# Kernel tuning notes

Measured on AMD Instinct MI355X. Metric: run time of the kernel, lower is better.

## Reference

```python
import jax, jax.numpy as jnp
import numpy as np

N = 50000        # total nodes (disjoint batch of graphs)
E = 800000       # total edges
F_IN = 8         # node feature dim
S = 6            # edge feature dim
H = 20           # ECC kernel-network hidden size (hidden_states)
N_OUT = 20       # ECC output channels (n_out=hidden_states)
G = 32           # GCN channels
D1 = 16          # first dense
N_GRAPHS = 512   # graphs in batch


def setup_inputs() -> dict:
    key = jax.random.key(0)
    ks = jax.random.split(key, 24)
    r = lambda k, sh, s: jax.random.normal(k, sh, dtype=jnp.float32) * s
    return {
        "x": r(ks[0], (N, F_IN), 1.0),
        "e": r(ks[1], (E, S), 1.0),
        "edge_index": jax.random.randint(ks[2], (2, E), 0, N, dtype=jnp.int32),
        "seg": jnp.sort(jax.random.randint(ks[3], (N,), 0, N_GRAPHS, dtype=jnp.int32)),
        # ECC kernel network: S -> H -> H -> F_IN*N_OUT
        "ecc_w1": r(ks[4], (S, H), 0.4), "ecc_b1": jnp.zeros((H,), jnp.float32),
        "ecc_w2": r(ks[5], (H, H), 0.2), "ecc_b2": jnp.zeros((H,), jnp.float32),
        "ecc_w3": r(ks[6], (H, F_IN * N_OUT), 0.2), "ecc_b3": jnp.zeros((F_IN * N_OUT,), jnp.float32),
        "ecc_root": r(ks[7], (F_IN, N_OUT), 0.3), "ecc_b": jnp.zeros((N_OUT,), jnp.float32),
        "gcn1_w": r(ks[8], (N_OUT, G), 0.2), "gcn1_b": jnp.zeros((G,), jnp.float32),
        "gcn2_w": r(ks[9], (G, G), 0.2), "gcn2_b": jnp.zeros((G,), jnp.float32),
        "d1_w": r(ks[10], (G, D1), 0.2), "d1_b": jnp.zeros((D1,), jnp.float32),
        "d2_w": r(ks[11], (D1, 1), 0.2), "d2_b": jnp.zeros((1,), jnp.float32),
    }


def reference(x, e, edge_index, seg,
              ecc_w1, ecc_b1, ecc_w2, ecc_b2, ecc_w3, ecc_b3, ecc_root, ecc_b,
              gcn1_w, gcn1_b, gcn2_w, gcn2_b, d1_w, d1_b, d2_w, d2_b):
    row, col = edge_index[0], edge_index[1]  # message col -> row

    # --- ECCConv: per-edge MLP produces an [F_IN, N_OUT] filter per edge ---
    h = jax.nn.relu(e @ ecc_w1 + ecc_b1)
    h = jax.nn.relu(h @ ecc_w2 + ecc_b2)
    w_edge = (h @ ecc_w3 + ecc_b3).reshape(E, F_IN, N_OUT)   # [E, F_in, F_out]
    msg = jnp.einsum('ef,efo->eo', x[col], w_edge)            # per-edge message
    agg = jax.ops.segment_sum(msg, row, num_segments=N)
    x1 = jax.nn.relu(agg + x @ ecc_root + ecc_b)              # root + bias + relu

    # --- GCN normalization from the edge list (A + I, symmetric norm) ---
    deg = jax.ops.segment_sum(jnp.ones((E,), x.dtype), row, num_segments=N) + 1.0
    dinv = jax.lax.rsqrt(deg)
    edge_norm = (dinv[row] * dinv[col])[:, None]
    self_norm = (dinv * dinv)[:, None]

    def gcn(hin, W, b):
        hw = hin @ W
        nmsg = jax.ops.segment_sum(edge_norm * hw[col], row, num_segments=N)
        return jax.nn.relu(nmsg + self_norm * hw + b)

    x2 = gcn(x1, gcn1_w, gcn1_b)
    x3 = gcn(x2, gcn2_w, gcn2_b)

    # --- GlobalSumPool over graph ids, then MLP head ---
    pooled = jax.ops.segment_sum(x3, seg, num_segments=N_GRAPHS)  # [n_graphs, G]
    out = (pooled @ d1_w + d1_b) @ d2_w + d2_b                    # [n_graphs, 1]
    return out
```

## Files before the change

kernel.cpp:

```cpp
#include <hip/hip_runtime.h>

#define S_DIM   6
#define H_DIM   20
#define F_INN   8
#define N_OUTC  20
#define G_DIM   32
#define D1_DIM  16
#define NGRAPH  512

__global__ __launch_bounds__(256) void loc_kernel(
    const int* __restrict__ ei, int E, int* __restrict__ cnt,
    int* __restrict__ loc)
{
    int i = blockIdx.x * 256 + threadIdx.x;
    if (i >= E) return;
    loc[i] = atomicAdd(&cnt[ei[i]], 1);
}

__global__ __launch_bounds__(256) void scanA_kernel(
    const int* __restrict__ deg, int N, int* __restrict__ bsum)
{
    int i = blockIdx.x * 256 + threadIdx.x;
    int v = (i < N) ? deg[i] : 0;
#pragma unroll
    for (int d = 1; d < 64; d <<= 1) v += __shfl_down(v, d, 64);
    __shared__ int ws[4];
    int wid = threadIdx.x >> 6;
    if ((threadIdx.x & 63) == 0) ws[wid] = v;
    __syncthreads();
    if (threadIdx.x == 0) bsum[blockIdx.x] = ws[0] + ws[1] + ws[2] + ws[3];
}

__global__ __launch_bounds__(256) void scanC_kernel(
    const int* __restrict__ deg, int N, const int* __restrict__ bsum, int nbl,
    int E, int* __restrict__ rowptr, float* __restrict__ dinv)
{
    __shared__ int ws[4];
    __shared__ int sboff;
    int t = threadIdx.x;

    {
        int v = (t < nbl && t < blockIdx.x) ? bsum[t] : 0;
#pragma unroll
        for (int d = 1; d < 64; d <<= 1) v += __shfl_down(v, d, 64);
        int wid = t >> 6;
        if ((t & 63) == 0) ws[wid] = v;
        __syncthreads();
        if (t == 0) sboff = ws[0] + ws[1] + ws[2] + ws[3];
        __syncthreads();
    }

    int i = blockIdx.x * 256 + t;
    int d0 = (i < N) ? deg[i] : 0;
    int v = d0;
#pragma unroll
    for (int d = 1; d < 64; d <<= 1) {
        int u = __shfl_up(v, d, 64);
        if ((t & 63) >= d) v += u;
    }
    __shared__ int ws2[4];
    int wid = t >> 6;
    if ((t & 63) == 63) ws2[wid] = v;
    __syncthreads();
    int woff = 0;
    for (int w = 0; w < wid; ++w) woff += ws2[w];
    if (i < N) {
        rowptr[i] = sboff + woff + v - d0;
        dinv[i] = rsqrtf((float)d0 + 1.0f);
    }
    if (blockIdx.x == 0 && t == 0) rowptr[N] = E;
}

__global__ __launch_bounds__(256) void build_kernel(
    const int* __restrict__ ei, int E, const int* __restrict__ rowptr,
    const int* __restrict__ loc,
    int* __restrict__ eid_at_slot, int* __restrict__ col_sorted)
{
    int i = blockIdx.x * 256 + threadIdx.x;
    if (i >= E) return;
    int p = rowptr[ei[i]] + loc[i];
    eid_at_slot[p] = i;
    col_sorted[p] = ei[E + i];
}

__global__ __launch_bounds__(256) void ecc_fused_kernel(
    const float* __restrict__ e, const float* __restrict__ x,
    const int* __restrict__ eid_at_slot, const int* __restrict__ col_sorted,
    const int* __restrict__ rowptr, int N, int E,
    const float* __restrict__ w1, const float* __restrict__ b1,
    const float* __restrict__ w2, const float* __restrict__ b2,
    const float* __restrict__ w3, const float* __restrict__ b3,
    float* __restrict__ agg)
{
    __shared__ float4 lmsg[5][257];
    __shared__ int rbounds[2];

    int t = threadIdx.x;
    int j0 = blockIdx.x * 256;
    int j = j0 + t;
    int jend = min(j0 + 256, E);

    if (t < 2) {
        int s = (t == 0) ? j0 : (jend - 1);
        int lo = 0, hi = N - 1;
        while (lo < hi) {
            int m = (lo + hi + 1) >> 1;
            if (rowptr[m] <= s) lo = m; else hi = m - 1;
        }
        rbounds[t] = lo;
    }

    if (j < E) {
        int i = eid_at_slot[j];
        int c = col_sorted[j];

        float ef[S_DIM];
#pragma unroll
        for (int s = 0; s < S_DIM; ++s) ef[s] = e[(size_t)i * S_DIM + s];

        float h1[H_DIM];
#pragma unroll
        for (int jj = 0; jj < H_DIM; ++jj) {
            float a = b1[jj];
#pragma unroll
            for (int s = 0; s < S_DIM; ++s) a = fmaf(ef[s], w1[s * H_DIM + jj], a);
            h1[jj] = fmaxf(a, 0.0f);
        }

        float h2[H_DIM];
#pragma unroll
        for (int jj = 0; jj < H_DIM; ++jj) {
            float a = b2[jj];
#pragma unroll
            for (int k = 0; k < H_DIM; ++k) a = fmaf(h1[k], w2[k * H_DIM + jj], a);
            h2[jj] = fmaxf(a, 0.0f);
        }

        const float4* xp = (const float4*)&x[(size_t)c * F_INN];
        float4 xa = xp[0], xb = xp[1];
        float xf[F_INN] = {xa.x, xa.y, xa.z, xa.w, xb.x, xb.y, xb.z, xb.w};

        float msg[N_OUTC];
#pragma unroll
        for (int o = 0; o < N_OUTC; ++o) msg[o] = 0.0f;

        for (int f = 0; f < F_INN; ++f) {
            float xv = xf[f];
#pragma unroll
            for (int o = 0; o < N_OUTC; ++o) {
                float w = b3[f * N_OUTC + o];
#pragma unroll
                for (int k = 0; k < H_DIM; ++k)
                    w = fmaf(h2[k], w3[k * (F_INN * N_OUTC) + f * N_OUTC + o], w);
                msg[o] = fmaf(xv, w, msg[o]);
            }
        }

        lmsg[0][t] = make_float4(msg[0],  msg[1],  msg[2],  msg[3]);
        lmsg[1][t] = make_float4(msg[4],  msg[5],  msg[6],  msg[7]);
        lmsg[2][t] = make_float4(msg[8],  msg[9],  msg[10], msg[11]);
        lmsg[3][t] = make_float4(msg[12], msg[13], msg[14], msg[15]);
        lmsg[4][t] = make_float4(msg[16], msg[17], msg[18], msg[19]);
    }
    __syncthreads();

    int r0 = rbounds[0], r1 = rbounds[1];
    int work = (r1 - r0 + 1) * 5;
    for (int w = t; w < work; w += 256) {
        int row = r0 + w / 5;
        int q = w - (w / 5) * 5;
        int a0 = rowptr[row], a1 = rowptr[row + 1];
        int s0 = max(a0, j0), s1 = min(a1, jend);
        float4 acc = make_float4(0.f, 0.f, 0.f, 0.f);
        for (int s = s0; s < s1; ++s) {
            float4 v = lmsg[q][s - j0];
            acc.x += v.x; acc.y += v.y; acc.z += v.z; acc.w += v.w;
        }
        float* dst = &agg[(size_t)row * N_OUTC + q * 4];
        if (a0 >= j0 && a1 <= jend) {
            *(float4*)dst = acc;
        } else {
            unsafeAtomicAdd(dst + 0, acc.x);
            unsafeAtomicAdd(dst + 1, acc.y);
            unsafeAtomicAdd(dst + 2, acc.z);
            unsafeAtomicAdd(dst + 3, acc.w);
        }
    }
}

__global__ __launch_bounds__(256) void node1_kernel(
    const float* __restrict__ agg, const float* __restrict__ x,
    const float* __restrict__ dinv, int N,
    const float* __restrict__ root, const float* __restrict__ eb,
    const float* __restrict__ g1w,
    float* __restrict__ hws1)
{
    int n = blockIdx.x * 256 + threadIdx.x;
    if (n >= N) return;

    const float4* xp = (const float4*)&x[(size_t)n * F_INN];
    float4 xa = xp[0], xb = xp[1];
    float xf[F_INN] = {xa.x, xa.y, xa.z, xa.w, xb.x, xb.y, xb.z, xb.w};

    float x1[N_OUTC];
#pragma unroll
    for (int o = 0; o < N_OUTC; ++o) {
        float a = agg[(size_t)n * N_OUTC + o] + eb[o];
#pragma unroll
        for (int f = 0; f < F_INN; ++f) a = fmaf(xf[f], root[f * N_OUTC + o], a);
        x1[o] = fmaxf(a, 0.0f);
    }

    float di = dinv[n];
    float4* hp = (float4*)&hws1[(size_t)n * G_DIM];
#pragma unroll
    for (int q = 0; q < G_DIM / 4; ++q) {
        float4 v;
        float* vv = &v.x;
#pragma unroll
        for (int u = 0; u < 4; ++u) {
            int g = q * 4 + u;
            float a = 0.0f;
#pragma unroll
            for (int o = 0; o < N_OUTC; ++o) a = fmaf(x1[o], g1w[o * G_DIM + g], a);
            vv[u] = a * di;
        }
        hp[q] = v;
    }
}

template<bool DO_MATMUL>
__global__ __launch_bounds__(256) void gcn_gather_kernel(
    const float* __restrict__ hws, const int* __restrict__ rowptr,
    const int* __restrict__ col_sorted, const float* __restrict__ dinv, int N,
    const float* __restrict__ bias, const float* __restrict__ w2,
    float* __restrict__ outbuf)
{
    __shared__ float x2s[32 * 33];
    __shared__ float w2s[G_DIM * G_DIM];

    int t = threadIdx.x;
    int nl = t >> 3;
    int q = t & 7;
    int n = blockIdx.x * 32 + nl;

    if (DO_MATMUL) {
        ((float4*)w2s)[t] = ((const float4*)w2)[t];
    }

    float4 xo = make_float4(0.f, 0.f, 0.f, 0.f);
    float di = 0.0f;
    if (n < N) {
        di = dinv[n];
        int j0 = rowptr[n], j1 = rowptr[n + 1];
        float4 s = *(const float4*)&hws[(size_t)n * G_DIM + q * 4];
        for (int j = j0; j < j1; ++j) {
            int c = col_sorted[j];
            float4 v = *(const float4*)&hws[(size_t)c * G_DIM + q * 4];
            s.x += v.x; s.y += v.y; s.z += v.z; s.w += v.w;
        }
        const float4 b4 = *(const float4*)&bias[q * 4];
        xo.x = fmaxf(fmaf(di, s.x, b4.x), 0.0f);
        xo.y = fmaxf(fmaf(di, s.y, b4.y), 0.0f);
        xo.z = fmaxf(fmaf(di, s.z, b4.z), 0.0f);
        xo.w = fmaxf(fmaf(di, s.w, b4.w), 0.0f);
    }

    if (DO_MATMUL) {
        x2s[nl * 33 + q * 4 + 0] = xo.x;
        x2s[nl * 33 + q * 4 + 1] = xo.y;
        x2s[nl * 33 + q * 4 + 2] = xo.z;
        x2s[nl * 33 + q * 4 + 3] = xo.w;
        __syncthreads();
        if (n < N) {
            float a0 = 0.f, a1 = 0.f, a2 = 0.f, a3 = 0.f;
            const float* xr = &x2s[nl * 33];
#pragma unroll
            for (int g = 0; g < G_DIM; ++g) {
                float xv = xr[g];
                a0 = fmaf(xv, w2s[g * G_DIM + q * 4 + 0], a0);
                a1 = fmaf(xv, w2s[g * G_DIM + q * 4 + 1], a1);
                a2 = fmaf(xv, w2s[g * G_DIM + q * 4 + 2], a2);
                a3 = fmaf(xv, w2s[g * G_DIM + q * 4 + 3], a3);
            }
            *(float4*)&outbuf[(size_t)n * G_DIM + q * 4] =
                make_float4(a0 * di, a1 * di, a2 * di, a3 * di);
        }
    } else {
        if (n < N)
            *(float4*)&outbuf[(size_t)n * G_DIM + q * 4] = xo;
    }
}

__global__ __launch_bounds__(256) void pool_head_kernel(
    const float* __restrict__ x3, const int* __restrict__ seg, int N,
    const float* __restrict__ d1w, const float* __restrict__ d1b,
    const float* __restrict__ d2w, const float* __restrict__ d2b,
    float* __restrict__ out)
{
    __shared__ float red[8][G_DIM];
    __shared__ float pvec[G_DIM];
    __shared__ int bounds[2];
    int g = blockIdx.x;
    int t = threadIdx.x;
    if (t < 2) {
        int target = g + t;
        int lo = 0, hi = N;
        while (lo < hi) {
            int m = (lo + hi) >> 1;
            if (seg[m] < target) lo = m + 1; else hi = m;
        }
        bounds[t] = lo;
    }
    __syncthreads();
    int n0 = bounds[0], n1 = bounds[1];
    int ch = t & (G_DIM - 1);
    int slice = t >> 5;
    float a = 0.0f;
    for (int n = n0 + slice; n < n1; n += 8)
        a += x3[(size_t)n * G_DIM + ch];
    red[slice][ch] = a;
    __syncthreads();
    if (slice == 0) {
        float s = red[0][ch];
#pragma unroll
        for (int k = 1; k < 8; ++k) s += red[k][ch];
        pvec[ch] = s;
    }
    __syncthreads();
    if (t < D1_DIM) {
        float tj = d1b[t];
#pragma unroll
        for (int gg = 0; gg < G_DIM; ++gg)
            tj = fmaf(pvec[gg], d1w[gg * D1_DIM + t], tj);
        float acc = tj * d2w[t];
#pragma unroll
        for (int d = 1; d < D1_DIM; d <<= 1) acc += __shfl_down(acc, d, 64);
        if (t == 0) out[g] = acc + d2b[0];
    }
}

extern "C" void kernel_launch(void* const* d_in, const int* in_sizes, int n_in,
                              void* d_out, int out_size, void* d_ws, size_t ws_size,
                              hipStream_t stream)
{
    const float* x    = (const float*)d_in[0];
    const float* e    = (const float*)d_in[1];
    const int*   ei   = (const int*)d_in[2];
    const int*   seg  = (const int*)d_in[3];
    const float* w1   = (const float*)d_in[4];
    const float* b1   = (const float*)d_in[5];
    const float* w2   = (const float*)d_in[6];
    const float* b2   = (const float*)d_in[7];
    const float* w3   = (const float*)d_in[8];
    const float* b3   = (const float*)d_in[9];
    const float* root = (const float*)d_in[10];
    const float* eb   = (const float*)d_in[11];
    const float* g1w  = (const float*)d_in[12];
    const float* g1b  = (const float*)d_in[13];
    const float* g2w  = (const float*)d_in[14];
    const float* g2b  = (const float*)d_in[15];
    const float* d1w  = (const float*)d_in[16];
    const float* d1b  = (const float*)d_in[17];
    const float* d2w  = (const float*)d_in[18];
    const float* d2b  = (const float*)d_in[19];

    const int N = in_sizes[3];
    const int E = in_sizes[1] / S_DIM;
    float* out = (float*)d_out;

    const int nbl = (N + 255) / 256;
    const int ebl = (E + 255) / 256;

    char* ws = (char*)d_ws;
    size_t off = 0;
    auto alloc = [&](size_t elems) -> char* {
        char* p = ws + off;
        off += ((elems * 4 + 15) & ~(size_t)15);
        return p;
    };
    int*   cnt        = (int*)  alloc(N);
    float* agg        = (float*)alloc((size_t)N * N_OUTC);
    size_t zero_bytes = off;
    int*   rowptr     = (int*)  alloc(N + 1);
    int*   bsum       = (int*)  alloc(nbl);
    float* dinv       = (float*)alloc(N);
    int*   loc        = (int*)  alloc(E);
    int*   eid_at_slot= (int*)  alloc(E);
    int*   col_sorted = (int*)  alloc(E);
    float* hws1       = (float*)alloc((size_t)N * G_DIM);
    float* hws2       = (float*)alloc((size_t)N * G_DIM);
    float* x3         = (float*)alloc((size_t)N * G_DIM);
    (void)ws_size;

    hipMemsetAsync(d_ws, 0, zero_bytes, stream);

    loc_kernel<<<ebl, 256, 0, stream>>>(ei, E, cnt, loc);
    scanA_kernel<<<nbl, 256, 0, stream>>>(cnt, N, bsum);
    scanC_kernel<<<nbl, 256, 0, stream>>>(cnt, N, bsum, nbl, E, rowptr, dinv);
    build_kernel<<<ebl, 256, 0, stream>>>(ei, E, rowptr, loc, eid_at_slot, col_sorted);
    ecc_fused_kernel<<<ebl, 256, 0, stream>>>(e, x, eid_at_slot, col_sorted,
                                              rowptr, N, E,
                                              w1, b1, w2, b2, w3, b3, agg);
    node1_kernel<<<nbl, 256, 0, stream>>>(agg, x, dinv, N, root, eb, g1w, hws1);
    gcn_gather_kernel<true><<<(N + 31) / 32, 256, 0, stream>>>(
        hws1, rowptr, col_sorted, dinv, N, g1b, g2w, hws2);
    gcn_gather_kernel<false><<<(N + 31) / 32, 256, 0, stream>>>(
        hws2, rowptr, col_sorted, dinv, N, g2b, nullptr, x3);
    pool_head_kernel<<<NGRAPH, 256, 0, stream>>>(x3, seg, N, d1w, d1b, d2w, d2b, out);
}
```

Measured before the change: 314.6 us.

## Compute ECC edge-filter contraction with bf16 MFMA instead of scalar FMAs

The per-edge third MLP layer and the x-weighted contraction are reformulated as one GEMM over the outer product h2⊗x (K=160, plus 8 bias terms) against a reshaped w3/b3 matrix. This matrix is run on 16x16x32 bf16 MFMA instructions. The weight B-fragments are staged through shared memory in bf16, and the message buffer is reused for the segmented reduction. This is meant to remove roughly 3200 scalar FMAs per edge, which dominated the kernel. The cost is bf16 rounding of the activations and weights, extra LDS traffic and syncs, and redundant B staging in every block.

```diff
diff --git a/kernel.cpp b/kernel.cpp
--- a/kernel.cpp
+++ b/kernel.cpp
@@ -8,6 +8,17 @@
 #define D1_DIM  16
 #define NGRAPH  512
 
+typedef short short8 __attribute__((ext_vector_type(8)));
+typedef float floatx4 __attribute__((ext_vector_type(4)));
+
+__device__ __forceinline__ unsigned short f2bf(float f) {
+    unsigned u = __float_as_uint(f);
+    return (unsigned short)((u + 0x8000u) >> 16);
+}
+__device__ __forceinline__ float bf2f(unsigned short s) {
+    return __uint_as_float(((unsigned)s) << 16);
+}
+
 __global__ __launch_bounds__(256) void loc_kernel(
     const int* __restrict__ ei, int E, int* __restrict__ cnt,
     int* __restrict__ loc)
@@ -38,7 +49,6 @@
     __shared__ int ws[4];
     __shared__ int sboff;
     int t = threadIdx.x;
-
     {
         int v = (t < nbl && t < blockIdx.x) ? bsum[t] : 0;
 #pragma unroll
@@ -83,7 +93,7 @@
     col_sorted[p] = ei[E + i];
 }
 
-__global__ __launch_bounds__(256) void ecc_fused_kernel(
+__global__ __launch_bounds__(256) void ecc_mfma_kernel(
     const float* __restrict__ e, const float* __restrict__ x,
     const int* __restrict__ eid_at_slot, const int* __restrict__ col_sorted,
     const int* __restrict__ rowptr, int N, int E,
@@ -92,13 +102,18 @@
     const float* __restrict__ w3, const float* __restrict__ b3,
     float* __restrict__ agg)
 {
-    __shared__ float4 lmsg[5][257];
+    __shared__ char ubuf[256 * N_OUTC * 4];
+    __shared__ unsigned short h2b[256][N_OUTC];
+    __shared__ unsigned short xb[256][F_INN];
     __shared__ int rbounds[2];
+
+    unsigned short* Bl = (unsigned short*)ubuf;
+    float* lmsg = (float*)ubuf;
 
     int t = threadIdx.x;
     int j0 = blockIdx.x * 256;
+    int jend = min(j0 + 256, E);
     int j = j0 + t;
-    int jend = min(j0 + 256, E);
 
     if (t < 2) {
         int s = (t == 0) ? j0 : (jend - 1);
@@ -110,6 +125,22 @@
         rbounds[t] = lo;
     }
 
+    for (int idx = t; idx < 6144; idx += 256) {
+        int jj   = idx & 7;
+        int n    = (idx >> 3) & 15;
+        int quad = (idx >> 7) & 3;
+        int nt   = (idx >> 9) & 1;
+        int s    = idx >> 10;
+        int K = 32 * s + quad * 8 + jj;
+        int o = n + 16 * nt;
+        float v = 0.0f;
+        if (o < N_OUTC) {
+            if (K < 160)      v = w3[(K >> 3) * 160 + (K & 7) * N_OUTC + o];
+            else if (K < 168) v = b3[(K - 160) * N_OUTC + o];
+        }
+        Bl[idx] = f2bf(v);
+    }
+
     if (j < E) {
         int i = eid_at_slot[j];
         int c = col_sorted[j];
@@ -137,43 +168,79 @@
         }
 
         const float4* xp = (const float4*)&x[(size_t)c * F_INN];
-        float4 xa = xp[0], xb = xp[1];
-        float xf[F_INN] = {xa.x, xa.y, xa.z, xa.w, xb.x, xb.y, xb.z, xb.w};
-
-        float msg[N_OUTC];
-#pragma unroll
-        for (int o = 0; o < N_OUTC; ++o) msg[o] = 0.0f;
-
-        for (int f = 0; f < F_INN; ++f) {
-            float xv = xf[f];
-#pragma unroll
-            for (int o = 0; o < N_OUTC; ++o) {
-                float w = b3[f * N_OUTC + o];
-#pragma unroll
-                for (int k = 0; k < H_DIM; ++k)
-                    w = fmaf(h2[k], w3[k * (F_INN * N_OUTC) + f * N_OUTC + o], w);
-                msg[o] = fmaf(xv, w, msg[o]);
+        float4 xa = xp[0], xb4 = xp[1];
+        float xf[F_INN] = {xa.x, xa.y, xa.z, xa.w, xb4.x, xb4.y, xb4.z, xb4.w};
+
+#pragma unroll
+        for (int o = 0; o < N_OUTC; ++o) h2b[t][o] = f2bf(h2[o]);
+#pragma unroll
+        for (int f = 0; f < F_INN; ++f) xb[t][f] = f2bf(xf[f]);
+    } else {
+#pragma unroll
+        for (int o = 0; o < N_OUTC; ++o) h2b[t][o] = 0;
+#pragma unroll
+        for (int f = 0; f < F_INN; ++f) xb[t][f] = 0;
+    }
+    __syncthreads();
+
+    int lane = t & 63;
+    int quad = lane >> 4;
+    int n = lane & 15;
+    short8 Bf[12];
+#pragma unroll
+    for (int s = 0; s < 6; ++s)
+#pragma unroll
+        for (int nt = 0; nt < 2; ++nt)
+            Bf[s * 2 + nt] = *(const short8*)&Bl[((((s * 2 + nt) * 4 + quad) * 16 + n) * 8)];
+    __syncthreads();
+
+    int w = t >> 6;
+#pragma unroll
+    for (int T = 0; T < 4; ++T) {
+        int base = w * 64 + T * 16;
+        int m = base + n;
+
+        const short8 xv8 = *(const short8*)&xb[m][0];
+        float xfl[F_INN];
+#pragma unroll
+        for (int jj = 0; jj < F_INN; ++jj) xfl[jj] = bf2f((unsigned short)xv8[jj]);
+
+        floatx4 acc0 = {0.f, 0.f, 0.f, 0.f};
+        floatx4 acc1 = {0.f, 0.f, 0.f, 0.f};
+#pragma unroll
+        for (int s = 0; s < 6; ++s) {
+            short8 A = {0, 0, 0, 0, 0, 0, 0, 0};
+            if (s < 5) {
+                float h = bf2f(h2b[m][4 * s + quad]);
+#pragma unroll
+                for (int jj = 0; jj < F_INN; ++jj)
+                    A[jj] = (short)f2bf(h * xfl[jj]);
+            } else if (quad == 0) {
+                A = xv8;
             }
-        }
-
-        lmsg[0][t] = make_float4(msg[0],  msg[1],  msg[2],  msg[3]);
-        lmsg[1][t] = make_float4(msg[4],  msg[5],  msg[6],  msg[7]);
-        lmsg[2][t] = make_float4(msg[8],  msg[9],  msg[10], msg[11]);
-        lmsg[3][t] = make_float4(msg[12], msg[13], msg[14], msg[15]);
-        lmsg[4][t] = make_float4(msg[16], msg[17], msg[18], msg[19]);
+            acc0 = __builtin_amdgcn_mfma_f32_16x16x32_bf16(A, Bf[s * 2 + 0], acc0, 0, 0, 0);
+            acc1 = __builtin_amdgcn_mfma_f32_16x16x32_bf16(A, Bf[s * 2 + 1], acc1, 0, 0, 0);
+        }
+
+#pragma unroll
+        for (int r = 0; r < 4; ++r) {
+            int row = base + quad * 4 + r;
+            lmsg[row * N_OUTC + n] = acc0[r];
+            if (n < 4) lmsg[row * N_OUTC + 16 + n] = acc1[r];
+        }
     }
     __syncthreads();
 
     int r0 = rbounds[0], r1 = rbounds[1];
     int work = (r1 - r0 + 1) * 5;
-    for (int w = t; w < work; w += 256) {
-        int row = r0 + w / 5;
-        int q = w - (w / 5) * 5;
+    for (int ww = t; ww < work; ww += 256) {
+        int row = r0 + ww / 5;
+        int q = ww - (ww / 5) * 5;
         int a0 = rowptr[row], a1 = rowptr[row + 1];
         int s0 = max(a0, j0), s1 = min(a1, jend);
         float4 acc = make_float4(0.f, 0.f, 0.f, 0.f);
         for (int s = s0; s < s1; ++s) {
-            float4 v = lmsg[q][s - j0];
+            const float4 v = *(const float4*)&lmsg[(s - j0) * N_OUTC + q * 4];
             acc.x += v.x; acc.y += v.y; acc.z += v.z; acc.w += v.w;
         }
         float* dst = &agg[(size_t)row * N_OUTC + q * 4];
@@ -328,12 +395,15 @@
         pvec[ch] = s;
     }
     __syncthreads();
-    if (t < D1_DIM) {
-        float tj = d1b[t];
-#pragma unroll
-        for (int gg = 0; gg < G_DIM; ++gg)
-            tj = fmaf(pvec[gg], d1w[gg * D1_DIM + t], tj);
-        float acc = tj * d2w[t];
+    if (t < 64) {
+        float acc = 0.0f;
+        if (t < D1_DIM) {
+            float tj = d1b[t];
+#pragma unroll
+            for (int gg = 0; gg < G_DIM; ++gg)
+                tj = fmaf(pvec[gg], d1w[gg * D1_DIM + t], tj);
+            acc = tj * d2w[t];
+        }
 #pragma unroll
         for (int d = 1; d < D1_DIM; d <<= 1) acc += __shfl_down(acc, d, 64);
         if (t == 0) out[g] = acc + d2b[0];
@@ -399,9 +469,9 @@
     scanA_kernel<<<nbl, 256, 0, stream>>>(cnt, N, bsum);
     scanC_kernel<<<nbl, 256, 0, stream>>>(cnt, N, bsum, nbl, E, rowptr, dinv);
     build_kernel<<<ebl, 256, 0, stream>>>(ei, E, rowptr, loc, eid_at_slot, col_sorted);
-    ecc_fused_kernel<<<ebl, 256, 0, stream>>>(e, x, eid_at_slot, col_sorted,
-                                              rowptr, N, E,
-                                              w1, b1, w2, b2, w3, b3, agg);
+    ecc_mfma_kernel<<<ebl, 256, 0, stream>>>(e, x, eid_at_slot, col_sorted,
+                                             rowptr, N, E,
+                                             w1, b1, w2, b2, w3, b3, agg);
     node1_kernel<<<nbl, 256, 0, stream>>>(agg, x, dinv, N, root, eb, g1w, hws1);
     gcn_gather_kernel<true><<<(N + 31) / 32, 256, 0, stream>>>(
         hws1, rowptr, col_sorted, dinv, N, g1b, g2w, hws2);
```

New measurement: 306.8 us. 2.5% less time.
